# Optimization experiments

Hardware: AMD Instinct MI355X
Metric: run time of the kernel (lower is better)

## Reference

```python
import jax, jax.numpy as jnp
import numpy as np

N_NODES = 100000
IN_CH, HID_CH, OUT_CH = 128, 128, 64
N_EDGES = 1600000


def _gcn_conv(x, W, b, src, dst, num_nodes):
    """PyG GCNConv with gcn_norm(add_self_loops=True): adds one self-loop per
    node to the given edge set, symmetric deg^-1/2 normalization, then
    gather-scale-scatter of the linearly transformed features."""
    loop = jnp.arange(num_nodes)
    s = jnp.concatenate([src, loop])
    d = jnp.concatenate([dst, loop])
    # degree over targets (flow source_to_target), edge weights = 1
    deg = jax.ops.segment_sum(jnp.ones_like(s, x.dtype), d, num_segments=num_nodes)
    dinv = jnp.where(deg > 0, deg ** -0.5, 0.0)
    norm = dinv[s] * dinv[d]                      # [E']
    h = x @ W                                     # [N, out]
    msg = h[s] * norm[:, None]                    # [E', out] gather + scale
    out = jax.ops.segment_sum(msg, d, num_segments=num_nodes)  # scatter-add
    return out + b


def setup_inputs() -> dict:
    key = jax.random.key(0)
    k = jax.random.split(key, 6)
    x = jax.random.normal(k[0], (N_NODES, IN_CH), dtype=jnp.float32)
    edge_index = jax.random.randint(k[1], (2, N_EDGES), 0, N_NODES, dtype=jnp.int64)
    # Glorot-scale params
    W1 = jax.random.normal(k[2], (IN_CH, HID_CH), dtype=jnp.float32) * (2.0 / (IN_CH + HID_CH)) ** 0.5
    b1 = jnp.zeros((HID_CH,), dtype=jnp.float32)
    W2 = jax.random.normal(k[3], (HID_CH, OUT_CH), dtype=jnp.float32) * (2.0 / (HID_CH + OUT_CH)) ** 0.5
    b2 = jnp.zeros((OUT_CH,), dtype=jnp.float32)
    return {"x": x, "edge_index": edge_index, "W1": W1, "b1": b1, "W2": W2, "b2": b2}


def reference(x, edge_index, W1, b1, W2, b2):
    num_nodes = x.shape[0]
    loop = jnp.arange(num_nodes, dtype=edge_index.dtype)
    # wrapper-level add_self_loops (GCNConv adds another internally)
    src = jnp.concatenate([edge_index[0], loop])
    dst = jnp.concatenate([edge_index[1], loop])
    h = _gcn_conv(x, W1, b1, src, dst, num_nodes)
    h = jax.nn.relu(h)
    h = _gcn_conv(h, W2, b2, src, dst, num_nodes)
    return jax.nn.log_softmax(h, axis=1)
```

## Files before the change

### kernel.cpp

```cpp
#include <hip/hip_runtime.h>
#include <cstdint>
#include <cstddef>

#define IN_CH 128
#define HID_CH 128
#define OUT_CH 64
#define BSH 8
#define PB 4096

typedef unsigned int uint32;
typedef unsigned char uchar;
typedef short bf16x8 __attribute__((ext_vector_type(8)));
typedef float f32x4 __attribute__((ext_vector_type(4)));
typedef float f32x2 __attribute__((ext_vector_type(2)));

static __device__ __forceinline__ unsigned short f2bf(float f) {
    uint32 u = __float_as_uint(f);
    u += 0x7fffu + ((u >> 16) & 1u);
    return (unsigned short)(u >> 16);
}
static __device__ __forceinline__ uchar f2fp8(float f) {
    int p = __builtin_amdgcn_cvt_pk_fp8_f32(f, f, 0, false);
    return (uchar)(p & 0xff);
}


__global__ __launch_bounds__(256) void bhist_wtrans(
    const int* __restrict__ dst, int* __restrict__ bcnt, int E, int NB, int gP,
    const float* __restrict__ W1, const float* __restrict__ W2,
    unsigned short* __restrict__ W1t, unsigned short* __restrict__ W2t) {
    if (blockIdx.x >= (uint32)gP) {
        int t = (blockIdx.x - gP) * 256 + threadIdx.x;
        if (t < 128 * 128) {
            int nc = t >> 7, k = t & 127;
            W1t[t] = f2bf(W1[k * 128 + nc]);
        }
        int u = t - 128 * 128;
        if (u >= 0 && u < 64 * 128) {
            int nc = u >> 7, k = u & 127;
            W2t[u] = f2bf(W2[k * 64 + nc]);
        }
        return;
    }
    __shared__ int h[512];
    int t = threadIdx.x;
    int e0 = blockIdx.x * PB;
    int cnt = min(PB, E - e0);
    for (int b = t; b < NB; b += 256) h[b] = 0;
    __syncthreads();
    for (int i = t; i < cnt; i += 256)
        atomicAdd(&h[dst[e0 + i] >> BSH], 1);
    __syncthreads();
    for (int b = t; b < NB; b += 256)
        if (h[b]) atomicAdd(&bcnt[b], h[b]);
}

__global__ void bscan(const int* __restrict__ bcnt, int* __restrict__ bbase,
                      int* __restrict__ bcur, int NB, int E) {
    __shared__ int s[512];
    int t = threadIdx.x;
    int v = (t < NB) ? bcnt[t] : 0;
    s[t] = v;
    __syncthreads();
    for (int o = 1; o < 512; o <<= 1) {
        int add = (t >= o) ? s[t - o] : 0;
        __syncthreads();
        s[t] += add;
        __syncthreads();
    }
    if (t < NB) { bbase[t] = s[t] - v; bcur[t] = 0; }
    if (t == 0) bbase[NB] = E;
}

__global__ __launch_bounds__(256) void part1(
    const int* __restrict__ src, const int* __restrict__ dst,
    const int* __restrict__ bbase, int* __restrict__ bcur,
    int2* __restrict__ pairBuf, int E, int NB) {
    __shared__ int2 pairs[PB];
    __shared__ int hist[512];
    __shared__ int base[512];
    int t = threadIdx.x;
    int e0 = blockIdx.x * PB;
    int cnt = min(PB, E - e0);
    for (int b = t; b < NB; b += 256) hist[b] = 0;
    __syncthreads();
    for (int i = t; i < cnt; i += 256) {
        int s = src[e0 + i], d = dst[e0 + i];
        pairs[i] = make_int2(s, d);
        atomicAdd(&hist[d >> BSH], 1);
    }
    __syncthreads();
    for (int b = t; b < NB; b += 256) {
        int h = hist[b];
        int gb = (h > 0) ? atomicAdd(&bcur[b], h) : 0;
        base[b] = bbase[b] + gb;
        hist[b] = 0;
    }
    __syncthreads();
    for (int i = t; i < cnt; i += 256) {
        int2 p = pairs[i];
        int b = p.y >> BSH;
        int q = base[b] + atomicAdd(&hist[b], 1);
        pairBuf[q] = p;
    }
}

__global__ __launch_bounds__(256) void bucket_build(
    const int2* __restrict__ pairBuf, const int* __restrict__ bbase,
    int* __restrict__ rowptr, int* __restrict__ deg, float* __restrict__ dinv,
    int* __restrict__ csr, int N) {
    __shared__ int cnt[256];
    __shared__ int loc[256];
    int b = blockIdx.x, t = threadIdx.x;
    int start = bbase[b], end = bbase[b + 1];
    cnt[t] = 0;
    __syncthreads();
    for (int i = start + t; i < end; i += 256)
        atomicAdd(&cnt[pairBuf[i].y & 255], 1);
    __syncthreads();
    int v = cnt[t];
    loc[t] = v;
    __syncthreads();
    for (int o = 1; o < 256; o <<= 1) {
        int add = (t >= o) ? loc[t - o] : 0;
        __syncthreads();
        loc[t] += add;
        __syncthreads();
    }
    int excl = loc[t] - v;
    int node = (b << BSH) + t;
    if (node < N) {
        rowptr[node] = start + excl;
        deg[node] = v;
        dinv[node] = rsqrtf((float)(v + 2));
    }
    __syncthreads();
    cnt[t] = excl;
    __syncthreads();
    for (int i = start + t; i < end; i += 256) {
        int2 p = pairBuf[i];
        int q = start + atomicAdd(&cnt[p.y & 255], 1);
        csr[q] = p.x;
    }
}


template <int OUT, bool AFP32>
__global__ __launch_bounds__(256, 4) void gemm_mfma(
    const void* __restrict__ Av, const unsigned short* __restrict__ Wt,
    const float* __restrict__ dinv, uchar* __restrict__ C, int n) {
    constexpr int WP = 136;
    constexpr int NT = OUT / 16;
    __shared__ unsigned short Ws[OUT * WP];

    const int t = threadIdx.x;
    const int row0 = blockIdx.x * 128;

    for (int i = t; i < OUT * 16; i += 256) {
        int rr = i >> 4, sq = i & 15;
        *(uint4*)&Ws[rr * WP + sq * 8] = *(const uint4*)(Wt + rr * 128 + sq * 8);
    }
    __syncthreads();

    const int w = t >> 6, l = t & 63;
    const int q = l >> 4, r16 = l & 15;
    const int mbase = w * 32;

    const int ra = row0 + mbase + r16;
    const int rb = ra + 16;
    const int rac = min(ra, n - 1);
    const int rbc = min(rb, n - 1);

    f32x4 acc0[NT], acc1[NT];
    for (int i = 0; i < NT; i++) {
        acc0[i] = (f32x4){0.f, 0.f, 0.f, 0.f};
        acc1[i] = (f32x4){0.f, 0.f, 0.f, 0.f};
    }

#pragma unroll
    for (int s = 0; s < 4; s++) {
        const int k0 = s * 32 + q * 8;
        bf16x8 a0, a1;
        if (AFP32) {
            const float* A = (const float*)Av;
            float4 v0 = *(const float4*)(A + (size_t)rac * 128 + k0);
            float4 v1 = *(const float4*)(A + (size_t)rac * 128 + k0 + 4);
            float4 u0 = *(const float4*)(A + (size_t)rbc * 128 + k0);
            float4 u1 = *(const float4*)(A + (size_t)rbc * 128 + k0 + 4);
            a0[0] = (short)f2bf(v0.x); a0[1] = (short)f2bf(v0.y);
            a0[2] = (short)f2bf(v0.z); a0[3] = (short)f2bf(v0.w);
            a0[4] = (short)f2bf(v1.x); a0[5] = (short)f2bf(v1.y);
            a0[6] = (short)f2bf(v1.z); a0[7] = (short)f2bf(v1.w);
            a1[0] = (short)f2bf(u0.x); a1[1] = (short)f2bf(u0.y);
            a1[2] = (short)f2bf(u0.z); a1[3] = (short)f2bf(u0.w);
            a1[4] = (short)f2bf(u1.x); a1[5] = (short)f2bf(u1.y);
            a1[6] = (short)f2bf(u1.z); a1[7] = (short)f2bf(u1.w);
        } else {
            const unsigned short* A = (const unsigned short*)Av;
            a0 = *(const bf16x8*)(A + (size_t)rac * 128 + k0);
            a1 = *(const bf16x8*)(A + (size_t)rbc * 128 + k0);
        }
#pragma unroll
        for (int nt = 0; nt < NT; nt++) {
            bf16x8 b = *(const bf16x8*)&Ws[(nt * 16 + r16) * WP + k0];
            acc0[nt] = __builtin_amdgcn_mfma_f32_16x16x32_bf16(a0, b, acc0[nt], 0, 0, 0);
            acc1[nt] = __builtin_amdgcn_mfma_f32_16x16x32_bf16(a1, b, acc1[nt], 0, 0, 0);
        }
    }

    float dva[4], dvb[4];
#pragma unroll
    for (int p = 0; p < 4; p++) {
        int rr = row0 + mbase + q * 4 + p;
        dva[p] = (rr < n) ? dinv[rr] : 0.f;
        dvb[p] = (rr + 16 < n) ? dinv[rr + 16] : 0.f;
    }

#pragma unroll
    for (int nt = 0; nt < NT; nt++) {
#pragma unroll
        for (int p = 0; p < 4; p++) {
            int rr = row0 + mbase + q * 4 + p;
            if (rr < n) C[(size_t)rr * OUT + nt * 16 + r16] = f2fp8(acc0[nt][p] * dva[p]);
            if (rr + 16 < n) C[(size_t)(rr + 16) * OUT + nt * 16 + r16] = f2fp8(acc1[nt][p] * dvb[p]);
        }
    }
}


__global__ __launch_bounds__(256) void agg_relu_128(
    const uchar* __restrict__ H, const int* __restrict__ csr,
    const int* __restrict__ rowptr, const int* __restrict__ deg,
    const float* __restrict__ dinv, const float* __restrict__ bias,
    unsigned short* __restrict__ out, int n) {
    int v = blockIdx.x * 16 + (threadIdx.x >> 4);
    int hl = threadIdx.x & 15;
    int gsel = threadIdx.x & 48;
    bool valid = v < n;
    int vc = valid ? v : 0;
    int base = rowptr[vc];
    int cnt = valid ? deg[vc] : 0;
    const uint32 co = (uint32)(hl * 8);

    f32x2 A0 = (f32x2){0.f, 0.f}, A1 = A0, A2 = A0, A3 = A0;
    f32x2 B0 = A0, B1 = A0, B2 = A0, B3 = A0;

#define ACC128(h, s0, s1, s2, s3)                                   \
    {                                                               \
        s0 += __builtin_amdgcn_cvt_pk_f32_fp8((h).x, false);        \
        s1 += __builtin_amdgcn_cvt_pk_f32_fp8((h).x, true);         \
        s2 += __builtin_amdgcn_cvt_pk_f32_fp8((h).y, false);        \
        s3 += __builtin_amdgcn_cvt_pk_f32_fp8((h).y, true);         \
    }

    for (int j0 = 0; j0 < cnt; j0 += 16) {
        int nj = min(16, cnt - j0);
        int ul = 0;
        if (hl < nj) ul = csr[base + j0 + hl];
        int j = 0;
        for (; j + 8 <= nj; j += 8) {
            int u0 = __shfl(ul, (j + 0) | gsel), u1 = __shfl(ul, (j + 1) | gsel);
            int u2 = __shfl(ul, (j + 2) | gsel), u3 = __shfl(ul, (j + 3) | gsel);
            int u4 = __shfl(ul, (j + 4) | gsel), u5 = __shfl(ul, (j + 5) | gsel);
            int u6 = __shfl(ul, (j + 6) | gsel), u7 = __shfl(ul, (j + 7) | gsel);
            uint2 h0 = *(const uint2*)(H + (((uint32)u0 << 7) + co));
            uint2 h1 = *(const uint2*)(H + (((uint32)u1 << 7) + co));
            uint2 h2 = *(const uint2*)(H + (((uint32)u2 << 7) + co));
            uint2 h3 = *(const uint2*)(H + (((uint32)u3 << 7) + co));
            uint2 h4 = *(const uint2*)(H + (((uint32)u4 << 7) + co));
            uint2 h5 = *(const uint2*)(H + (((uint32)u5 << 7) + co));
            uint2 h6 = *(const uint2*)(H + (((uint32)u6 << 7) + co));
            uint2 h7 = *(const uint2*)(H + (((uint32)u7 << 7) + co));
            ACC128(h0, A0, A1, A2, A3);
            ACC128(h1, B0, B1, B2, B3);
            ACC128(h2, A0, A1, A2, A3);
            ACC128(h3, B0, B1, B2, B3);
            ACC128(h4, A0, A1, A2, A3);
            ACC128(h5, B0, B1, B2, B3);
            ACC128(h6, A0, A1, A2, A3);
            ACC128(h7, B0, B1, B2, B3);
        }
        for (; j + 4 <= nj; j += 4) {
            int u0 = __shfl(ul, (j + 0) | gsel), u1 = __shfl(ul, (j + 1) | gsel);
            int u2 = __shfl(ul, (j + 2) | gsel), u3 = __shfl(ul, (j + 3) | gsel);
            uint2 h0 = *(const uint2*)(H + (((uint32)u0 << 7) + co));
            uint2 h1 = *(const uint2*)(H + (((uint32)u1 << 7) + co));
            uint2 h2 = *(const uint2*)(H + (((uint32)u2 << 7) + co));
            uint2 h3 = *(const uint2*)(H + (((uint32)u3 << 7) + co));
            ACC128(h0, A0, A1, A2, A3);
            ACC128(h1, B0, B1, B2, B3);
            ACC128(h2, A0, A1, A2, A3);
            ACC128(h3, B0, B1, B2, B3);
        }
        for (; j < nj; j++) {
            int u = __shfl(ul, j | gsel);
            uint2 h = *(const uint2*)(H + (((uint32)u << 7) + co));
            ACC128(h, A0, A1, A2, A3);
        }
    }
#undef ACC128

    if (valid) {
        float dv = dinv[vc];
        uint2 hv = *(const uint2*)(H + (((uint32)vc << 7) + co));
        f32x2 s0 = __builtin_amdgcn_cvt_pk_f32_fp8(hv.x, false);
        f32x2 s1 = __builtin_amdgcn_cvt_pk_f32_fp8(hv.x, true);
        f32x2 s2 = __builtin_amdgcn_cvt_pk_f32_fp8(hv.y, false);
        f32x2 s3 = __builtin_amdgcn_cvt_pk_f32_fp8(hv.y, true);
        const f32x2* bp = (const f32x2*)(bias + hl * 8);
        f32x2 e0 = dv * ((A0 + B0) + 2.f * s0) + bp[0];
        f32x2 e1 = dv * ((A1 + B1) + 2.f * s1) + bp[1];
        f32x2 e2 = dv * ((A2 + B2) + 2.f * s2) + bp[2];
        f32x2 e3 = dv * ((A3 + B3) + 2.f * s3) + bp[3];
        float o0 = fmaxf(e0[0], 0.f), o1 = fmaxf(e0[1], 0.f);
        float o2 = fmaxf(e1[0], 0.f), o3 = fmaxf(e1[1], 0.f);
        float o4 = fmaxf(e2[0], 0.f), o5 = fmaxf(e2[1], 0.f);
        float o6 = fmaxf(e3[0], 0.f), o7 = fmaxf(e3[1], 0.f);
        uint4 pk;
        pk.x = (uint32)f2bf(o0) | ((uint32)f2bf(o1) << 16);
        pk.y = (uint32)f2bf(o2) | ((uint32)f2bf(o3) << 16);
        pk.z = (uint32)f2bf(o4) | ((uint32)f2bf(o5) << 16);
        pk.w = (uint32)f2bf(o6) | ((uint32)f2bf(o7) << 16);
        *(uint4*)(out + (size_t)vc * 128 + hl * 8) = pk;
    }
}

__global__ __launch_bounds__(256) void agg_lsm_64(
    const uchar* __restrict__ H, const int* __restrict__ csr,
    const int* __restrict__ rowptr, const int* __restrict__ deg,
    const float* __restrict__ dinv, const float* __restrict__ bias,
    float* __restrict__ out, int n) {
    int v = blockIdx.x * 16 + (threadIdx.x >> 4);
    int hl = threadIdx.x & 15;
    int gsel = threadIdx.x & 48;
    bool valid = v < n;
    int vc = valid ? v : 0;
    int base = rowptr[vc];
    int cnt = valid ? deg[vc] : 0;
    const uint32 co = (uint32)(hl * 4);

    f32x2 A0 = (f32x2){0.f, 0.f}, A1 = A0, B0 = A0, B1 = A0;

#define ACC64(h, s0, s1)                                            \
    {                                                               \
        s0 += __builtin_amdgcn_cvt_pk_f32_fp8((h), false);          \
        s1 += __builtin_amdgcn_cvt_pk_f32_fp8((h), true);           \
    }

    for (int j0 = 0; j0 < cnt; j0 += 16) {
        int nj = min(16, cnt - j0);
        int ul = 0;
        if (hl < nj) ul = csr[base + j0 + hl];
        int j = 0;
        for (; j + 8 <= nj; j += 8) {
            int u0 = __shfl(ul, (j + 0) | gsel), u1 = __shfl(ul, (j + 1) | gsel);
            int u2 = __shfl(ul, (j + 2) | gsel), u3 = __shfl(ul, (j + 3) | gsel);
            int u4 = __shfl(ul, (j + 4) | gsel), u5 = __shfl(ul, (j + 5) | gsel);
            int u6 = __shfl(ul, (j + 6) | gsel), u7 = __shfl(ul, (j + 7) | gsel);
            uint32 h0 = *(const uint32*)(H + (((uint32)u0 << 6) + co));
            uint32 h1 = *(const uint32*)(H + (((uint32)u1 << 6) + co));
            uint32 h2 = *(const uint32*)(H + (((uint32)u2 << 6) + co));
            uint32 h3 = *(const uint32*)(H + (((uint32)u3 << 6) + co));
            uint32 h4 = *(const uint32*)(H + (((uint32)u4 << 6) + co));
            uint32 h5 = *(const uint32*)(H + (((uint32)u5 << 6) + co));
            uint32 h6 = *(const uint32*)(H + (((uint32)u6 << 6) + co));
            uint32 h7 = *(const uint32*)(H + (((uint32)u7 << 6) + co));
            ACC64(h0, A0, A1);
            ACC64(h1, B0, B1);
            ACC64(h2, A0, A1);
            ACC64(h3, B0, B1);
            ACC64(h4, A0, A1);
            ACC64(h5, B0, B1);
            ACC64(h6, A0, A1);
            ACC64(h7, B0, B1);
        }
        for (; j + 4 <= nj; j += 4) {
            int u0 = __shfl(ul, (j + 0) | gsel), u1 = __shfl(ul, (j + 1) | gsel);
            int u2 = __shfl(ul, (j + 2) | gsel), u3 = __shfl(ul, (j + 3) | gsel);
            uint32 h0 = *(const uint32*)(H + (((uint32)u0 << 6) + co));
            uint32 h1 = *(const uint32*)(H + (((uint32)u1 << 6) + co));
            uint32 h2 = *(const uint32*)(H + (((uint32)u2 << 6) + co));
            uint32 h3 = *(const uint32*)(H + (((uint32)u3 << 6) + co));
            ACC64(h0, A0, A1);
            ACC64(h1, B0, B1);
            ACC64(h2, A0, A1);
            ACC64(h3, B0, B1);
        }
        for (; j < nj; j++) {
            int u = __shfl(ul, j | gsel);
            uint32 h = *(const uint32*)(H + (((uint32)u << 6) + co));
            ACC64(h, A0, A1);
        }
    }
#undef ACC64

    float dv = dinv[vc];
    uint32 hv = *(const uint32*)(H + (((uint32)vc << 6) + co));
    f32x2 s0 = __builtin_amdgcn_cvt_pk_f32_fp8(hv, false);
    f32x2 s1 = __builtin_amdgcn_cvt_pk_f32_fp8(hv, true);
    const f32x2* bp = (const f32x2*)(bias + hl * 4);
    f32x2 w0 = dv * ((A0 + B0) + 2.f * s0) + bp[0];
    f32x2 w1 = dv * ((A1 + B1) + 2.f * s1) + bp[1];
    float v0 = w0[0], v1 = w0[1], v2 = w1[0], v3 = w1[1];
    float m = fmaxf(fmaxf(v0, v1), fmaxf(v2, v3));
    for (int o = 8; o > 0; o >>= 1) m = fmaxf(m, __shfl_xor(m, o));
    float e = (__expf(v0 - m) + __expf(v1 - m)) + (__expf(v2 - m) + __expf(v3 - m));
    for (int o = 8; o > 0; o >>= 1) e += __shfl_xor(e, o);
    float ls = m + __logf(e);
    if (valid)
        *(float4*)(out + (size_t)vc * 64 + hl * 4) =
            make_float4(v0 - ls, v1 - ls, v2 - ls, v3 - ls);
}


extern "C" void kernel_launch(void* const* d_in, const int* in_sizes, int n_in,
                              void* d_out, int out_size, void* d_ws, size_t ws_size,
                              hipStream_t stream) {
    const float* x  = (const float*)d_in[0];
    const int*   ei = (const int*)d_in[1];
    const float* W1 = (const float*)d_in[2];
    const float* b1 = (const float*)d_in[3];
    const float* W2 = (const float*)d_in[4];
    const float* b2 = (const float*)d_in[5];
    float* out = (float*)d_out;

    const int N = in_sizes[0] / IN_CH;
    const int E = in_sizes[1] / 2;
    const int* src = ei;
    const int* dst = ei + E;
    const int NB = (N + 255) >> BSH;

    char* w = (char*)d_ws;
    size_t off = 0;
    auto alloc = [&](size_t bytes) -> char* {
        char* p = w + off;
        off = (off + bytes + 255) & ~(size_t)255;
        return p;
    };
    int*   deg    = (int*)alloc((size_t)N * 4);
    int*   rowptr = (int*)alloc((size_t)N * 4);
    int*   bcnt   = (int*)alloc(512 * 4);
    int*   bbase  = (int*)alloc(513 * 4);
    int*   bcur   = (int*)alloc(512 * 4);
    float* dinv   = (float*)alloc((size_t)N * 4);
    int*   csr    = (int*)alloc((size_t)E * 4);
    unsigned short* W1t = (unsigned short*)alloc(128 * 128 * 2);
    unsigned short* W2t = (unsigned short*)alloc(64 * 128 * 2);
    uchar* H1  = (uchar*)alloc((size_t)N * HID_CH);
    unsigned short* A1b = (unsigned short*)alloc((size_t)N * HID_CH * 2);
    uchar* H2  = H1;
    int2*  pairBuf = (int2*)A1b;

    hipMemsetAsync(bcnt, 0, 512 * 4, stream);

    int gP = (E + PB - 1) / PB;

    bhist_wtrans<<<gP + 96, 256, 0, stream>>>(dst, bcnt, E, NB, gP, W1, W2, W1t, W2t);
    bscan<<<1, 512, 0, stream>>>(bcnt, bbase, bcur, NB, E);
    part1<<<gP, 256, 0, stream>>>(src, dst, bbase, bcur, pairBuf, E, NB);
    bucket_build<<<NB, 256, 0, stream>>>(pairBuf, bbase, rowptr, deg, dinv, csr, N);

    gemm_mfma<128, true><<<(N + 127) / 128, 256, 0, stream>>>(x, W1t, dinv, H1, N);
    agg_relu_128<<<(N + 15) / 16, 256, 0, stream>>>(H1, csr, rowptr, deg, dinv, b1, A1b, N);
    gemm_mfma<64, false><<<(N + 127) / 128, 256, 0, stream>>>(A1b, W2t, dinv, H2, N);
    agg_lsm_64<<<(N + 15) / 16, 256, 0, stream>>>(H2, csr, rowptr, deg, dinv, b2, out, N);
}
```

Measured before the change: 246.7 us.

## Drop LDS weight staging in GEMM, read weights from global/L2, halve rows per block

The MFMA GEMM no longer copies the transposed weight matrix into shared memory or needs the block barrier. B fragments are loaded straight from global memory, where they should stay cache-resident. Each wave now handles 16 rows instead of 32, with all A fragments loaded up front to give more memory-level parallelism, and the grid doubles to match. The trade-off is more global/L2 traffic for weights per output and less reuse of each B fragment across rows, in exchange for no LDS setup and higher occupancy.

After: 272.3 us. +10.4%, slower.

```diff
diff --git a/kernel.cpp b/kernel.cpp
--- a/kernel.cpp
+++ b/kernel.cpp
@@ -146,83 +146,68 @@
 
 
 template <int OUT, bool AFP32>
-__global__ __launch_bounds__(256, 4) void gemm_mfma(
+__global__ __launch_bounds__(256) void gemm_mfma(
     const void* __restrict__ Av, const unsigned short* __restrict__ Wt,
     const float* __restrict__ dinv, uchar* __restrict__ C, int n) {
-    constexpr int WP = 136;
     constexpr int NT = OUT / 16;
-    __shared__ unsigned short Ws[OUT * WP];
 
     const int t = threadIdx.x;
-    const int row0 = blockIdx.x * 128;
-
-    for (int i = t; i < OUT * 16; i += 256) {
-        int rr = i >> 4, sq = i & 15;
-        *(uint4*)&Ws[rr * WP + sq * 8] = *(const uint4*)(Wt + rr * 128 + sq * 8);
-    }
-    __syncthreads();
-
     const int w = t >> 6, l = t & 63;
     const int q = l >> 4, r16 = l & 15;
-    const int mbase = w * 32;
-
-    const int ra = row0 + mbase + r16;
-    const int rb = ra + 16;
+    const int row0 = blockIdx.x * 64 + w * 16;
+    const int ra = row0 + r16;
     const int rac = min(ra, n - 1);
-    const int rbc = min(rb, n - 1);
-
-    f32x4 acc0[NT], acc1[NT];
-    for (int i = 0; i < NT; i++) {
-        acc0[i] = (f32x4){0.f, 0.f, 0.f, 0.f};
-        acc1[i] = (f32x4){0.f, 0.f, 0.f, 0.f};
+
+    f32x4 acc[NT];
+#pragma unroll
+    for (int i = 0; i < NT; i++) acc[i] = (f32x4){0.f, 0.f, 0.f, 0.f};
+
+    bf16x8 afr[4];
+    if (AFP32) {
+        const float* A = (const float*)Av + (size_t)rac * 128;
+        float4 v[8];
+#pragma unroll
+        for (int s = 0; s < 4; s++) {
+            int k0 = s * 32 + q * 8;
+            v[2 * s]     = *(const float4*)(A + k0);
+            v[2 * s + 1] = *(const float4*)(A + k0 + 4);
+        }
+#pragma unroll
+        for (int s = 0; s < 4; s++) {
+            afr[s][0] = (short)f2bf(v[2 * s].x);     afr[s][1] = (short)f2bf(v[2 * s].y);
+            afr[s][2] = (short)f2bf(v[2 * s].z);     afr[s][3] = (short)f2bf(v[2 * s].w);
+            afr[s][4] = (short)f2bf(v[2 * s + 1].x); afr[s][5] = (short)f2bf(v[2 * s + 1].y);
+            afr[s][6] = (short)f2bf(v[2 * s + 1].z); afr[s][7] = (short)f2bf(v[2 * s + 1].w);
+        }
+    } else {
+        const unsigned short* A = (const unsigned short*)Av + (size_t)rac * 128;
+#pragma unroll
+        for (int s = 0; s < 4; s++)
+            afr[s] = *(const bf16x8*)(A + s * 32 + q * 8);
     }
 
 #pragma unroll
     for (int s = 0; s < 4; s++) {
         const int k0 = s * 32 + q * 8;
-        bf16x8 a0, a1;
-        if (AFP32) {
-            const float* A = (const float*)Av;
-            float4 v0 = *(const float4*)(A + (size_t)rac * 128 + k0);
-            float4 v1 = *(const float4*)(A + (size_t)rac * 128 + k0 + 4);
-            float4 u0 = *(const float4*)(A + (size_t)rbc * 128 + k0);
-            float4 u1 = *(const float4*)(A + (size_t)rbc * 128 + k0 + 4);
-            a0[0] = (short)f2bf(v0.x); a0[1] = (short)f2bf(v0.y);
-            a0[2] = (short)f2bf(v0.z); a0[3] = (short)f2bf(v0.w);
-            a0[4] = (short)f2bf(v1.x); a0[5] = (short)f2bf(v1.y);
-            a0[6] = (short)f2bf(v1.z); a0[7] = (short)f2bf(v1.w);
-            a1[0] = (short)f2bf(u0.x); a1[1] = (short)f2bf(u0.y);
-            a1[2] = (short)f2bf(u0.z); a1[3] = (short)f2bf(u0.w);
-            a1[4] = (short)f2bf(u1.x); a1[5] = (short)f2bf(u1.y);
-            a1[6] = (short)f2bf(u1.z); a1[7] = (short)f2bf(u1.w);
-        } else {
-            const unsigned short* A = (const unsigned short*)Av;
-            a0 = *(const bf16x8*)(A + (size_t)rac * 128 + k0);
-            a1 = *(const bf16x8*)(A + (size_t)rbc * 128 + k0);
-        }
 #pragma unroll
         for (int nt = 0; nt < NT; nt++) {
-            bf16x8 b = *(const bf16x8*)&Ws[(nt * 16 + r16) * WP + k0];
-            acc0[nt] = __builtin_amdgcn_mfma_f32_16x16x32_bf16(a0, b, acc0[nt], 0, 0, 0);
-            acc1[nt] = __builtin_amdgcn_mfma_f32_16x16x32_bf16(a1, b, acc1[nt], 0, 0, 0);
-        }
-    }
-
-    float dva[4], dvb[4];
+            bf16x8 b = *(const bf16x8*)(Wt + (size_t)(nt * 16 + r16) * 128 + k0);
+            acc[nt] = __builtin_amdgcn_mfma_f32_16x16x32_bf16(afr[s], b, acc[nt], 0, 0, 0);
+        }
+    }
+
+    float dva[4];
 #pragma unroll
     for (int p = 0; p < 4; p++) {
-        int rr = row0 + mbase + q * 4 + p;
+        int rr = row0 + q * 4 + p;
         dva[p] = (rr < n) ? dinv[rr] : 0.f;
-        dvb[p] = (rr + 16 < n) ? dinv[rr + 16] : 0.f;
-    }
-
+    }
 #pragma unroll
     for (int nt = 0; nt < NT; nt++) {
 #pragma unroll
         for (int p = 0; p < 4; p++) {
-            int rr = row0 + mbase + q * 4 + p;
-            if (rr < n) C[(size_t)rr * OUT + nt * 16 + r16] = f2fp8(acc0[nt][p] * dva[p]);
-            if (rr + 16 < n) C[(size_t)(rr + 16) * OUT + nt * 16 + r16] = f2fp8(acc1[nt][p] * dvb[p]);
+            int rr = row0 + q * 4 + p;
+            if (rr < n) C[(size_t)rr * OUT + nt * 16 + r16] = f2fp8(acc[nt][p] * dva[p]);
         }
     }
 }
@@ -460,8 +445,8 @@
     part1<<<gP, 256, 0, stream>>>(src, dst, bbase, bcur, pairBuf, E, NB);
     bucket_build<<<NB, 256, 0, stream>>>(pairBuf, bbase, rowptr, deg, dinv, csr, N);
 
-    gemm_mfma<128, true><<<(N + 127) / 128, 256, 0, stream>>>(x, W1t, dinv, H1, N);
+    gemm_mfma<128, true><<<(N + 63) / 64, 256, 0, stream>>>(x, W1t, dinv, H1, N);
     agg_relu_128<<<(N + 15) / 16, 256, 0, stream>>>(H1, csr, rowptr, deg, dinv, b1, A1b, N);
-    gemm_mfma<64, false><<<(N + 127) / 128, 256, 0, stream>>>(A1b, W2t, dinv, H2, N);
+    gemm_mfma<64, false><<<(N + 63) / 64, 256, 0, stream>>>(A1b, W2t, dinv, H2, N);
     agg_lsm_64<<<(N + 15) / 16, 256, 0, stream>>>(H2, csr, rowptr, deg, dinv, b2, out, N);
 }
```
